# Performance work log

Measured on AMD Instinct MI355X. Metric: run time of the kernel, lower is better.

Reference implementation:

```python
import jax, jax.numpy as jnp
import numpy as np

B, F, D, K = 4096, 1, 256, 65536

def setup_inputs() -> dict:
    key = jax.random.key(0)
    k1, k2, k3 = jax.random.split(key, 3)
    xhat_BFD = jax.random.normal(k1, (B, F, D), dtype=jnp.float32)
    x_BD = jax.random.normal(k2, (B * F, D), dtype=jnp.float32)
    centroids = jax.random.normal(k3, (K, D), dtype=jnp.float32)
    return {"xhat_BFD": xhat_BFD, "x_BD": x_BD, "centroids": centroids}

def reference(xhat_BFD, x_BD, centroids):
    c_sq_K = jnp.sum(centroids * centroids, axis=-1)            # [K]
    dists_BK = c_sq_K[None, :] - 2.0 * (x_BD @ centroids.T)     # [B*F, K] (GEMM-based distances)
    codes_B = jnp.argmin(dists_BK, axis=-1)                      # [B*F]
    quant_x_BD = centroids[codes_B]                              # embedding lookup of winners
    Bb, Ff, Dd = xhat_BFD.shape
    xhat_next = quant_x_BD.reshape(Bb, Ff, Dd)
    codes_BF = codes_B.reshape(Bb, Ff)
    return xhat_next, codes_BF
```

## Files before the change

kernel.cpp:

```cpp
#include <hip/hip_runtime.h>
#include <hip/hip_bf16.h>
#include <math.h>


#define DDIM 256
#define QTILE 128
#define STSZ 8192
#define QCAP 48
#define F16_MINN 6.103515625e-5f

typedef __attribute__((ext_vector_type(8))) _Float16 half8;
typedef __attribute__((ext_vector_type(4))) _Float16 half4;
typedef __attribute__((ext_vector_type(4))) float f32x4;

__device__ __forceinline__ void gl_lds16(const void* g, void* l) {
  __builtin_amdgcn_global_load_lds((const __attribute__((address_space(1))) void*)g,
                                   (__attribute__((address_space(3))) void*)l, 16, 0, 0);
}

__device__ __forceinline__ unsigned fkey(float d) {
  unsigned ud = __float_as_uint(d);
  return ud ^ (((int)ud < 0) ? 0xFFFFFFFFu : 0x80000000u);
}

__global__ __launch_bounds__(256) void splitc_kernel(const float* __restrict__ in,
                                                     _Float16* __restrict__ o0,
                                                     float* __restrict__ c_sq) {
  int i = blockIdx.x * 256 + threadIdx.x;
  int lane = (int)threadIdx.x & 63;
  float4 v = ((const float4*)in)[i];
  float vv[4] = {v.x, v.y, v.z, v.w};
  half4 h0;
#pragma unroll
  for (int e = 0; e < 4; ++e)
    h0[e] = (fabsf(vv[e]) < F16_MINN) ? (_Float16)0.f : (_Float16)vv[e];
  *(half4*)(o0 + (size_t)i * 4) = h0;
  float s = fmaf(v.x, v.x, fmaf(v.y, v.y, fmaf(v.z, v.z, v.w * v.w)));
#pragma unroll
  for (int off = 32; off > 0; off >>= 1) s += __shfl_down(s, off, 64);
  if (lane == 0) c_sq[i >> 6] = s;
}

__global__ __launch_bounds__(256) void splitx_kernel(const float* __restrict__ in,
                                                     _Float16* __restrict__ o0, int n4,
                                                     unsigned* __restrict__ ctl) {
  if (blockIdx.x == 0 && threadIdx.x < 64) ctl[threadIdx.x] = 0u;
  int i = blockIdx.x * 256 + threadIdx.x;
  if (i >= n4) return;
  float4 v = ((const float4*)in)[i];
  float vv[4] = {v.x, v.y, v.z, v.w};
  half4 h0;
#pragma unroll
  for (int e = 0; e < 4; ++e)
    h0[e] = (fabsf(vv[e]) < F16_MINN) ? (_Float16)0.f : (_Float16)vv[e];
  *(half4*)(o0 + (size_t)i * 4) = h0;
}

__global__ __launch_bounds__(256) void cmax_kernel(const float* __restrict__ c_sq,
                                                   unsigned* __restrict__ ctl) {
  __shared__ float red[4];
  int t = blockIdx.x * 256 + (int)threadIdx.x;
  float4 v = ((const float4*)c_sq)[t];
  float m = fmaxf(fmaxf(v.x, v.y), fmaxf(v.z, v.w));
#pragma unroll
  for (int off = 32; off > 0; off >>= 1) m = fmaxf(m, __shfl_down(m, off, 64));
  int lane = (int)threadIdx.x & 63, w = (int)threadIdx.x >> 6;
  if (lane == 0) red[w] = m;
  __syncthreads();
  if (threadIdx.x == 0) {
    m = fmaxf(fmaxf(red[0], red[1]), fmaxf(red[2], red[3]));
    atomicMax(&ctl[32], __float_as_uint(m));
  }
}

__global__ __launch_bounds__(1024) void scan_kernel(
    const _Float16* __restrict__ x0, const _Float16* __restrict__ c0,
    const float* __restrict__ c_sq, float* __restrict__ dm,
    float* __restrict__ pm) {
  __shared__ __align__(16) _Float16 As0[32768];
  __shared__ float pmred[2048];

  const int kc = blockIdx.x, qb = blockIdx.y;
  const int tid = (int)threadIdx.x;
  const int lane = tid & 63, w = tid >> 6;
  const int col = lane & 15, quad = lane >> 4;
  const int qrow0 = qb * QTILE;

  pmred[tid] = INFINITY;
  pmred[tid + 1024] = INFINITY;

#pragma unroll
  for (int i = 0; i < 4; ++i) {
    int u = i * 1024 + tid;
    int q = u & 127, s = u >> 7;
    gl_lds16(x0 + (size_t)(qrow0 + q) * DDIM + s * 8, As0 + (size_t)u * 8);
  }
  __syncthreads();

  for (int ct = 0; ct < STSZ / 512; ++ct) {
    const int cbase = kc * STSZ + ct * 512 + w * 32;
    f32x4 acc[2][8];
#pragma unroll
    for (int cm = 0; cm < 2; ++cm)
#pragma unroll
      for (int qn = 0; qn < 8; ++qn) acc[cm][qn] = (f32x4)0.0f;

#pragma unroll 2
    for (int kt = 0; kt < 8; ++kt) {
      const int k0 = kt * 32;
      half8 cf[2];
#pragma unroll
      for (int cm = 0; cm < 2; ++cm)
        cf[cm] = *(const half8*)(c0 + (size_t)(cbase + cm * 16 + col) * DDIM + k0 + quad * 8);
#pragma unroll
      for (int qn = 0; qn < 8; ++qn) {
        half8 qf = *(const half8*)(As0 + (size_t)(((kt * 4 + quad) * QTILE) + qn * 16 + col) * 8);
#pragma unroll
        for (int cm = 0; cm < 2; ++cm)
          acc[cm][qn] = __builtin_amdgcn_mfma_f32_16x16x32_f16(cf[cm], qf, acc[cm][qn], 0, 0, 0);
      }
    }

    f32x4 csv[2];
#pragma unroll
    for (int cm = 0; cm < 2; ++cm)
      csv[cm] = *(const f32x4*)(c_sq + cbase + cm * 16 + quad * 4);
    const int grp = kc * (STSZ / 32) + ct * 16 + w;
    float* dmg = dm + (size_t)grp * 4096 + qrow0;
#pragma unroll
    for (int qn = 0; qn < 8; ++qn) {
      float mq = INFINITY;
#pragma unroll
      for (int cm = 0; cm < 2; ++cm)
#pragma unroll
        for (int rg = 0; rg < 4; ++rg)
          mq = fminf(mq, fmaf(-2.0f, acc[cm][qn][rg], csv[cm][rg]));
      mq = fminf(mq, __shfl_xor(mq, 16, 64));
      mq = fminf(mq, __shfl_xor(mq, 32, 64));
      if (quad == 0) {
        dmg[qn * 16 + col] = mq;
        const int pi = w * 128 + qn * 16 + col;
        pmred[pi] = fminf(pmred[pi], mq);
      }
    }
  }

  __syncthreads();
  if (tid < 128) {
    float m = INFINITY;
#pragma unroll
    for (int i = 0; i < 16; ++i) m = fminf(m, pmred[i * 128 + tid]);
    pm[(size_t)kc * 4096 + qrow0 + tid] = m;
  }
}

__global__ __launch_bounds__(256) void tq_kernel(const float* __restrict__ pm,
                                                 const float* __restrict__ x,
                                                 const unsigned* __restrict__ ctl,
                                                 float* __restrict__ T,
                                                 unsigned* __restrict__ cnt) {
  int q = blockIdx.x * 256 + (int)threadIdx.x;
  float M = INFINITY;
#pragma unroll
  for (int i = 0; i < 8; ++i) M = fminf(M, pm[i * 4096 + q]);
  float xsq = 0.f;
  const float4* xr = (const float4*)(x + (size_t)q * DDIM);
#pragma unroll 8
  for (int i = 0; i < 64; ++i) {
    float4 v = xr[i];
    xsq = fmaf(v.x, v.x, fmaf(v.y, v.y, fmaf(v.z, v.z, fmaf(v.w, v.w, xsq))));
  }
  float cmaxsq = __uint_as_float(ctl[32]);
  T[q] = M + 0.0078125f * sqrtf(xsq * cmaxsq) + 1.0f;
  cnt[q] = 0u;
}

__global__ __launch_bounds__(256) void emit_kernel(const float* __restrict__ dm,
                                                   const float* __restrict__ T,
                                                   unsigned short* __restrict__ cand,
                                                   unsigned* __restrict__ cnt) {
  int qc = blockIdx.x & 15, gc = blockIdx.x >> 4;
  int q = qc * 256 + (int)threadIdx.x;
  float t = T[q];
  for (int g = gc * 128; g < gc * 128 + 128; ++g)
    if (dm[(size_t)g * 4096 + q] <= t) {
      unsigned slot = atomicAdd(&cnt[q], 1u);
      if (slot < QCAP) cand[(size_t)q * QCAP + slot] = (unsigned short)g;
    }
}

__global__ __launch_bounds__(256) void rescore_final_kernel(
    const unsigned short* __restrict__ cand, const unsigned* __restrict__ cnt,
    const float* __restrict__ x, const float* __restrict__ cent,
    const float* __restrict__ c_sq, float* __restrict__ out) {
  __shared__ unsigned long long red[4];
  const int q = blockIdx.x;
  const int w = (int)threadIdx.x >> 6, lane = (int)threadIdx.x & 63;
  const unsigned n = cnt[q];
  unsigned long long best = 0xFFFFFFFFFFFFFFFFull;
  if (n >= 1 && n <= QCAP) {
    int dh = (lane & 1) * 128;
    const float4* xr = (const float4*)(x + (size_t)q * DDIM + dh);
    for (unsigned sl = (unsigned)w; sl < n; sl += 4) {
      int g = (int)cand[(size_t)q * QCAP + sl];
      int c = g * 32 + (lane >> 1);
      const float4* cr = (const float4*)(cent + (size_t)c * DDIM + dh);
      float s = 0.f;
#pragma unroll
      for (int i = 0; i < 32; ++i) {
        float4 a = xr[i], bb = cr[i];
        s = fmaf(a.x, bb.x, fmaf(a.y, bb.y, fmaf(a.z, bb.z, fmaf(a.w, bb.w, s))));
      }
      s += __shfl_xor(s, 1, 64);
      float d = (lane & 1) ? INFINITY : fmaf(-2.0f, s, c_sq[c]);
      unsigned long long pkv = ((unsigned long long)fkey(d) << 32) | (unsigned)c;
      if (pkv < best) best = pkv;
    }
  } else {
    const float4* xr = (const float4*)(x + (size_t)q * DDIM);
    for (int c = (w << 6) + lane; c < 65536; c += 256) {
      const float4* cr = (const float4*)(cent + (size_t)c * DDIM);
      float s = 0.f;
#pragma unroll 16
      for (int i = 0; i < 64; ++i) {
        float4 a = xr[i], bb = cr[i];
        s = fmaf(a.x, bb.x, fmaf(a.y, bb.y, fmaf(a.z, bb.z, fmaf(a.w, bb.w, s))));
      }
      float d = fmaf(-2.0f, s, c_sq[c]);
      unsigned long long pkv = ((unsigned long long)fkey(d) << 32) | (unsigned)c;
      if (pkv < best) best = pkv;
    }
  }
#pragma unroll
  for (int off = 1; off < 64; off <<= 1) {
    unsigned long long o = __shfl_xor(best, off, 64);
    if (o < best) best = o;
  }
  if (lane == 0) red[w] = best;
  __syncthreads();
  if (w == 0) {
    unsigned long long b = red[lane & 3];
#pragma unroll
    for (int off = 1; off < 4; off <<= 1) {
      unsigned long long o = __shfl_xor(b, off, 64);
      if (o < b) b = o;
    }
    int idx = (int)(unsigned)(b & 0xFFFFFFFFu);
    float4 v = ((const float4*)cent)[(size_t)idx * 64 + lane];
    ((float4*)out)[(size_t)q * 64 + lane] = v;
    if (lane == 0) out[(size_t)4096 * DDIM + q] = (float)idx;
  }
}

extern "C" void kernel_launch(void* const* d_in, const int* in_sizes, int n_in,
                              void* d_out, int out_size, void* d_ws, size_t ws_size,
                              hipStream_t stream) {
  const float* x    = (const float*)d_in[1];
  const float* cent = (const float*)d_in[2];
  float* out = (float*)d_out;
  char* ws = (char*)d_ws;

  const size_t OFF_C0   = 0;
  const size_t OFF_X0   = 33554432;
  const size_t OFF_CSQ  = 35651584;
  const size_t OFF_CTL  = 35913728;
  const size_t OFF_DM   = 35913984;
  const size_t OFF_PM   = 69468416;
  const size_t OFF_T    = 69730560;
  const size_t OFF_CNT  = 69746944;
  const size_t OFF_CAND = 69763328;
  const size_t NEED     = 72089600;
  if (ws_size < NEED) return;

  _Float16* c0 = (_Float16*)(ws + OFF_C0);
  _Float16* x0 = (_Float16*)(ws + OFF_X0);
  float* c_sq = (float*)(ws + OFF_CSQ);
  unsigned* ctl = (unsigned*)(ws + OFF_CTL);
  float* dm = (float*)(ws + OFF_DM);
  float* pm = (float*)(ws + OFF_PM);
  float* T  = (float*)(ws + OFF_T);
  unsigned* cnt = (unsigned*)(ws + OFF_CNT);
  unsigned short* cand = (unsigned short*)(ws + OFF_CAND);

  splitc_kernel<<<16384, 256, 0, stream>>>(cent, c0, c_sq);
  splitx_kernel<<<1024, 256, 0, stream>>>(x, x0, 4096 * 256 / 4, ctl);
  cmax_kernel<<<64, 256, 0, stream>>>(c_sq, ctl);
  scan_kernel<<<dim3(8, 32), 1024, 0, stream>>>(x0, c0, c_sq, dm, pm);
  tq_kernel<<<16, 256, 0, stream>>>(pm, x, ctl, T, cnt);
  emit_kernel<<<256, 256, 0, stream>>>(dm, T, cand, cnt);
  rescore_final_kernel<<<4096, 256, 0, stream>>>(cand, cnt, x, cent, c_sq, out);
}
```

Before: 355.2 us.

## Fuse threshold, candidate emission and rescoring into one finish kernel

Replaces the threshold, emit and rescore/gather kernels with a single kernel that handles 16 queries per 512-thread block. Thresholds, candidate counts and candidate lists now live in shared memory instead of global workspace. This removes two launches, the global atomics and the global round trips for the candidate lists. The trade-off is less parallelism: only 256 blocks run, each wave rescoring two queries serially, and the fallback full scan now uses one wave per query instead of four.

```diff
diff --git a/kernel.cpp b/kernel.cpp
--- a/kernel.cpp
+++ b/kernel.cpp
@@ -154,101 +154,116 @@
   }
 }
 
-__global__ __launch_bounds__(256) void tq_kernel(const float* __restrict__ pm,
-                                                 const float* __restrict__ x,
-                                                 const unsigned* __restrict__ ctl,
-                                                 float* __restrict__ T,
-                                                 unsigned* __restrict__ cnt) {
-  int q = blockIdx.x * 256 + (int)threadIdx.x;
-  float M = INFINITY;
-#pragma unroll
-  for (int i = 0; i < 8; ++i) M = fminf(M, pm[i * 4096 + q]);
-  float xsq = 0.f;
-  const float4* xr = (const float4*)(x + (size_t)q * DDIM);
-#pragma unroll 8
-  for (int i = 0; i < 64; ++i) {
-    float4 v = xr[i];
-    xsq = fmaf(v.x, v.x, fmaf(v.y, v.y, fmaf(v.z, v.z, fmaf(v.w, v.w, xsq))));
-  }
-  float cmaxsq = __uint_as_float(ctl[32]);
-  T[q] = M + 0.0078125f * sqrtf(xsq * cmaxsq) + 1.0f;
-  cnt[q] = 0u;
-}
-
-__global__ __launch_bounds__(256) void emit_kernel(const float* __restrict__ dm,
-                                                   const float* __restrict__ T,
-                                                   unsigned short* __restrict__ cand,
-                                                   unsigned* __restrict__ cnt) {
-  int qc = blockIdx.x & 15, gc = blockIdx.x >> 4;
-  int q = qc * 256 + (int)threadIdx.x;
-  float t = T[q];
-  for (int g = gc * 128; g < gc * 128 + 128; ++g)
-    if (dm[(size_t)g * 4096 + q] <= t) {
-      unsigned slot = atomicAdd(&cnt[q], 1u);
-      if (slot < QCAP) cand[(size_t)q * QCAP + slot] = (unsigned short)g;
-    }
-}
-
-__global__ __launch_bounds__(256) void rescore_final_kernel(
-    const unsigned short* __restrict__ cand, const unsigned* __restrict__ cnt,
-    const float* __restrict__ x, const float* __restrict__ cent,
-    const float* __restrict__ c_sq, float* __restrict__ out) {
-  __shared__ unsigned long long red[4];
-  const int q = blockIdx.x;
-  const int w = (int)threadIdx.x >> 6, lane = (int)threadIdx.x & 63;
-  const unsigned n = cnt[q];
-  unsigned long long best = 0xFFFFFFFFFFFFFFFFull;
-  if (n >= 1 && n <= QCAP) {
-    int dh = (lane & 1) * 128;
-    const float4* xr = (const float4*)(x + (size_t)q * DDIM + dh);
-    for (unsigned sl = (unsigned)w; sl < n; sl += 4) {
-      int g = (int)cand[(size_t)q * QCAP + sl];
-      int c = g * 32 + (lane >> 1);
-      const float4* cr = (const float4*)(cent + (size_t)c * DDIM + dh);
-      float s = 0.f;
-#pragma unroll
-      for (int i = 0; i < 32; ++i) {
-        float4 a = xr[i], bb = cr[i];
-        s = fmaf(a.x, bb.x, fmaf(a.y, bb.y, fmaf(a.z, bb.z, fmaf(a.w, bb.w, s))));
-      }
-      s += __shfl_xor(s, 1, 64);
-      float d = (lane & 1) ? INFINITY : fmaf(-2.0f, s, c_sq[c]);
-      unsigned long long pkv = ((unsigned long long)fkey(d) << 32) | (unsigned)c;
-      if (pkv < best) best = pkv;
-    }
-  } else {
-    const float4* xr = (const float4*)(x + (size_t)q * DDIM);
-    for (int c = (w << 6) + lane; c < 65536; c += 256) {
-      const float4* cr = (const float4*)(cent + (size_t)c * DDIM);
-      float s = 0.f;
+__global__ __launch_bounds__(512) void finish_kernel(
+    const float* __restrict__ pm, const float* __restrict__ x,
+    const unsigned* __restrict__ ctl, const float* __restrict__ dm,
+    const float* __restrict__ cent, const float* __restrict__ c_sq,
+    float* __restrict__ out) {
+  __shared__ float Tl[16];
+  __shared__ unsigned cnt16[16];
+  __shared__ unsigned short candL[16][QCAP];
+  __shared__ float xred[16][33];
+  __shared__ unsigned long long bestL[16];
+
+  const int t = (int)threadIdx.x;
+  const int w = t >> 6, lane = t & 63;
+  const int q0 = (int)blockIdx.x * 16;
+
+  {
+    int qi = t >> 5, ch = t & 31;
+    const float4* xr = (const float4*)(x + (size_t)(q0 + qi) * DDIM + ch * 8);
+    float s = 0.f;
+#pragma unroll
+    for (int j = 0; j < 2; ++j) {
+      float4 v = xr[j];
+      s = fmaf(v.x, v.x, fmaf(v.y, v.y, fmaf(v.z, v.z, fmaf(v.w, v.w, s))));
+    }
+    xred[qi][ch] = s;
+    if (t < 16) cnt16[t] = 0u;
+  }
+  __syncthreads();
+  if (t < 16) {
+    float xsq = 0.f;
+#pragma unroll
+    for (int i = 0; i < 32; ++i) xsq += xred[t][i];
+    float M = INFINITY;
+#pragma unroll
+    for (int i = 0; i < 8; ++i) M = fminf(M, pm[i * 4096 + q0 + t]);
+    float cmaxsq = __uint_as_float(ctl[32]);
+    Tl[t] = M + 0.0078125f * sqrtf(xsq * cmaxsq) + 1.0f;
+  }
+  __syncthreads();
+
+  {
+    const int qi = t & 15, g0 = t >> 4;
+    const float Tq = Tl[qi];
+#pragma unroll 4
+    for (int i = 0; i < 64; ++i) {
+      int g = g0 + i * 32;
+      float v = dm[(size_t)g * 4096 + q0 + qi];
+      if (v <= Tq) {
+        unsigned slot = atomicAdd(&cnt16[qi], 1u);
+        if (slot < QCAP) candL[qi][slot] = (unsigned short)g;
+      }
+    }
+  }
+  __syncthreads();
+
+#pragma unroll
+  for (int k = 0; k < 2; ++k) {
+    const int qi = w + k * 8;
+    const unsigned n = cnt16[qi];
+    unsigned long long bq = 0xFFFFFFFFFFFFFFFFull;
+    if (n >= 1 && n <= QCAP) {
+      int dh = (lane & 1) * 128;
+      const float4* xr = (const float4*)(x + (size_t)(q0 + qi) * DDIM + dh);
+      for (unsigned sl = 0; sl < n; ++sl) {
+        int g = (int)candL[qi][sl];
+        int c = g * 32 + (lane >> 1);
+        const float4* cr = (const float4*)(cent + (size_t)c * DDIM + dh);
+        float s = 0.f;
+#pragma unroll
+        for (int i = 0; i < 32; ++i) {
+          float4 a = xr[i], bb = cr[i];
+          s = fmaf(a.x, bb.x, fmaf(a.y, bb.y, fmaf(a.z, bb.z, fmaf(a.w, bb.w, s))));
+        }
+        s += __shfl_xor(s, 1, 64);
+        float d = (lane & 1) ? INFINITY : fmaf(-2.0f, s, c_sq[c]);
+        unsigned long long pkv = ((unsigned long long)fkey(d) << 32) | (unsigned)c;
+        if (pkv < bq) bq = pkv;
+      }
+    } else {
+      const float4* xr = (const float4*)(x + (size_t)(q0 + qi) * DDIM);
+      for (int c = lane; c < 65536; c += 64) {
+        const float4* cr = (const float4*)(cent + (size_t)c * DDIM);
+        float s = 0.f;
 #pragma unroll 16
-      for (int i = 0; i < 64; ++i) {
-        float4 a = xr[i], bb = cr[i];
-        s = fmaf(a.x, bb.x, fmaf(a.y, bb.y, fmaf(a.z, bb.z, fmaf(a.w, bb.w, s))));
-      }
-      float d = fmaf(-2.0f, s, c_sq[c]);
-      unsigned long long pkv = ((unsigned long long)fkey(d) << 32) | (unsigned)c;
-      if (pkv < best) best = pkv;
-    }
-  }
-#pragma unroll
-  for (int off = 1; off < 64; off <<= 1) {
-    unsigned long long o = __shfl_xor(best, off, 64);
-    if (o < best) best = o;
-  }
-  if (lane == 0) red[w] = best;
-  __syncthreads();
-  if (w == 0) {
-    unsigned long long b = red[lane & 3];
-#pragma unroll
-    for (int off = 1; off < 4; off <<= 1) {
-      unsigned long long o = __shfl_xor(b, off, 64);
-      if (o < b) b = o;
-    }
-    int idx = (int)(unsigned)(b & 0xFFFFFFFFu);
-    float4 v = ((const float4*)cent)[(size_t)idx * 64 + lane];
-    ((float4*)out)[(size_t)q * 64 + lane] = v;
-    if (lane == 0) out[(size_t)4096 * DDIM + q] = (float)idx;
+        for (int i = 0; i < 64; ++i) {
+          float4 a = xr[i], bb = cr[i];
+          s = fmaf(a.x, bb.x, fmaf(a.y, bb.y, fmaf(a.z, bb.z, fmaf(a.w, bb.w, s))));
+        }
+        float d = fmaf(-2.0f, s, c_sq[c]);
+        unsigned long long pkv = ((unsigned long long)fkey(d) << 32) | (unsigned)c;
+        if (pkv < bq) bq = pkv;
+      }
+    }
+#pragma unroll
+    for (int off = 1; off < 64; off <<= 1) {
+      unsigned long long o = __shfl_xor(bq, off, 64);
+      if (o < bq) bq = o;
+    }
+    if (lane == 0) bestL[qi] = bq;
+  }
+  __syncthreads();
+
+  {
+    int qi = t >> 5, part = t & 31;
+    int idx = (int)(unsigned)(bestL[qi] & 0xFFFFFFFFu);
+    const float4* cr = (const float4*)(cent + (size_t)idx * DDIM);
+    float4* orow = (float4*)(out + (size_t)(q0 + qi) * DDIM);
+#pragma unroll
+    for (int j = 0; j < 2; ++j) orow[part * 2 + j] = cr[part * 2 + j];
+    if (part == 0) out[(size_t)4096 * DDIM + q0 + qi] = (float)idx;
   }
 }
 
@@ -266,9 +281,6 @@
   const size_t OFF_CTL  = 35913728;
   const size_t OFF_DM   = 35913984;
   const size_t OFF_PM   = 69468416;
-  const size_t OFF_T    = 69730560;
-  const size_t OFF_CNT  = 69746944;
-  const size_t OFF_CAND = 69763328;
   const size_t NEED     = 72089600;
   if (ws_size < NEED) return;
 
@@ -278,15 +290,10 @@
   unsigned* ctl = (unsigned*)(ws + OFF_CTL);
   float* dm = (float*)(ws + OFF_DM);
   float* pm = (float*)(ws + OFF_PM);
-  float* T  = (float*)(ws + OFF_T);
-  unsigned* cnt = (unsigned*)(ws + OFF_CNT);
-  unsigned short* cand = (unsigned short*)(ws + OFF_CAND);
 
   splitc_kernel<<<16384, 256, 0, stream>>>(cent, c0, c_sq);
   splitx_kernel<<<1024, 256, 0, stream>>>(x, x0, 4096 * 256 / 4, ctl);
   cmax_kernel<<<64, 256, 0, stream>>>(c_sq, ctl);
   scan_kernel<<<dim3(8, 32), 1024, 0, stream>>>(x0, c0, c_sq, dm, pm);
-  tq_kernel<<<16, 256, 0, stream>>>(pm, x, ctl, T, cnt);
-  emit_kernel<<<256, 256, 0, stream>>>(dm, T, cand, cnt);
-  rescore_final_kernel<<<4096, 256, 0, stream>>>(cand, cnt, x, cent, c_sq, out);
-}
+  finish_kernel<<<256, 512, 0, stream>>>(pm, x, ctl, dm, cent, c_sq, out);
+}
```

Result: faster. 326.1 us (-8.2%).
